# Kernel tuning notes

Hardware: AMD Instinct MI355X
Metric: run time of the kernel (lower is better)

Reference implementation:

```python
import jax, jax.numpy as jnp
import numpy as np

N_EMBD = 1024
COND = 1024
N_HEAD = 16
B, N, NTOK = 4, 2048, 2048


def setup_inputs() -> dict:
    key = jax.random.key(0)
    ks = jax.random.split(key, 10)
    s = 0.02
    return {
        "x": jax.random.normal(ks[0], (B, N, N_EMBD), jnp.float32),
        "encoder_output": jax.random.normal(ks[1], (B, NTOK, COND), jnp.float32),
        "Wq": jax.random.normal(ks[2], (N_EMBD, N_EMBD), jnp.float32) * s,
        "bq": jnp.zeros((N_EMBD,), jnp.float32),
        "Wk": jax.random.normal(ks[3], (N_EMBD, COND), jnp.float32) * s,
        "bk": jnp.zeros((N_EMBD,), jnp.float32),
        "Wv": jax.random.normal(ks[4], (N_EMBD, COND), jnp.float32) * s,
        "bv": jnp.zeros((N_EMBD,), jnp.float32),
        "Wp": jax.random.normal(ks[5], (N_EMBD, N_EMBD), jnp.float32) * s,
        "bp": jnp.zeros((N_EMBD,), jnp.float32),
    }


def reference(x, encoder_output, Wq, bq, Wk, bk, Wv, bv, Wp, bp):
    Bx, Nx, C = x.shape
    H = N_HEAD
    D = C // H
    # projections (torch Linear: y = x @ W^T + b)
    q = (x @ Wq.T + bq).reshape(Bx, Nx, H, D)               # b n h d
    k = (encoder_output @ Wk.T + bk).reshape(Bx, -1, H, D)  # b t h d
    v = (encoder_output @ Wv.T + bv).reshape(Bx, -1, H, D)
    scale = 1.0 / jnp.sqrt(jnp.asarray(D, x.dtype))
    att = jnp.einsum("bnhd,bthd->bhnt", q, k) * scale
    att = jax.nn.softmax(att, axis=-1)
    y = jnp.einsum("bhnt,bthd->bnhd", att, v).reshape(Bx, Nx, C)
    y = y @ Wp.T + bp  # dropout is identity at inference (p effectively 0)
    return y
```

## Files before the change

kernel.cpp:

```cpp
#include <hip/hip_runtime.h>

typedef short bf16x8 __attribute__((ext_vector_type(8)));
typedef float f32x4 __attribute__((ext_vector_type(4)));
typedef unsigned int u32x2 __attribute__((ext_vector_type(2)));

#define AS1 __attribute__((address_space(1)))
#define AS3 __attribute__((address_space(3)))

__device__ __forceinline__ void gld16(void* lds, const void* g) {
  __builtin_amdgcn_global_load_lds((const AS1 unsigned int*)g,
                                   (AS3 unsigned int*)lds, 16, 0, 0);
}

__device__ __forceinline__ unsigned short f2bf(float f) {
  union { float f; unsigned int u; } c; c.f = f;
  return (unsigned short)((c.u + 0x7FFFu + ((c.u >> 16) & 1u)) >> 16);
}

__device__ __forceinline__ unsigned short cvt1(float x) {
  unsigned int r;
  asm("v_cvt_pk_bf16_f32 %0, %1, %1" : "=v"(r) : "v"(x));
  return (unsigned short)r;
}

__device__ __forceinline__ unsigned int cvtpk(float lo, float hi) {
  unsigned int r;
  asm("v_cvt_pk_bf16_f32 %0, %1, %2" : "=v"(r) : "v"(lo), "v"(hi));
  return r;
}

__global__ void cvt_kernel(const float4* __restrict__ in0,
                           const float4* __restrict__ in1,
                           ushort4* __restrict__ out0,
                           ushort4* __restrict__ out1, int n4) {
  const float4* in = blockIdx.y ? in1 : in0;
  ushort4* out = blockIdx.y ? out1 : out0;
  int i = blockIdx.x * blockDim.x + threadIdx.x;
  int stride = gridDim.x * blockDim.x;
  for (; i < n4; i += stride) {
    float4 v = in[i];
    ushort4 o;
    o.x = f2bf(v.x); o.y = f2bf(v.y); o.z = f2bf(v.z); o.w = f2bf(v.w);
    out[i] = o;
  }
}

__global__ void cvtw_kernel(const float4* w0, const float4* w1,
                            const float4* w2, const float4* w3,
                            ushort4* o0, ushort4* o1, ushort4* o2, ushort4* o3,
                            int n4) {
  const float4* in; ushort4* out;
  switch (blockIdx.y) {
    case 0: in = w0; out = o0; break;
    case 1: in = w1; out = o1; break;
    case 2: in = w2; out = o2; break;
    default: in = w3; out = o3; break;
  }
  int i = blockIdx.x * blockDim.x + threadIdx.x;
  int stride = gridDim.x * blockDim.x;
  for (; i < n4; i += stride) {
    float4 v = in[i];
    ushort4 o;
    o.x = f2bf(v.x); o.y = f2bf(v.y); o.z = f2bf(v.z); o.w = f2bf(v.w);
    out[i] = o;
  }
}

__global__ __launch_bounds__(256) void gemm_qkv_kernel(
    const unsigned short* __restrict__ Xb,
    const unsigned short* __restrict__ Eb,
    const unsigned short* __restrict__ Wqb,
    const unsigned short* __restrict__ Wkb,
    const unsigned short* __restrict__ Wvb,
    const float* __restrict__ bq,
    const float* __restrict__ bk,
    const float* __restrict__ bv,
    unsigned short* __restrict__ Qw,
    unsigned short* __restrict__ Kw,
    unsigned short* __restrict__ VTw,
    float qscale)
{
  __shared__ alignas(16) unsigned short As[2][4 * 128 * 8];
  __shared__ alignas(16) unsigned short Bs[2][4 * 128 * 8];

  const int bid = blockIdx.x;
  const int o = (bid & 7) * 192 + (bid >> 3);
  const int xx = o % 24;
  const int yy = o / 24;
  const int sec = xx >> 3;
  const int nx = xx & 7;

  const unsigned short* A = (sec == 0) ? Xb : Eb;
  const unsigned short* W = (sec == 0) ? Wqb : (sec == 1) ? Wkb : Wvb;
  const float* bias = (sec == 0) ? bq : (sec == 1) ? bk : bv;

  const int K = 1024, N = 1024;
  const int tid = threadIdx.x;
  const int lane = tid & 63;
  const int w = tid >> 6;
  const int wr = (w >> 1) * 64;
  const int wc = (w & 1) * 64;
  const int lrow = lane & 15;
  const int lk = lane >> 4;
  const long m0 = (long)yy * 128;
  const long n0 = (long)nx * 128;

  f32x4 acc[4][4] = {};

  const int c0 = tid, c1 = tid + 256;
  const unsigned short* Ag0 = A + (m0 + (c0 & 127)) * (long)K + (c0 >> 7) * 8;
  const unsigned short* Ag1 = A + (m0 + (c1 & 127)) * (long)K + (c1 >> 7) * 8;
  const unsigned short* Wg0 = W + (n0 + (c0 & 127)) * (long)K + (c0 >> 7) * 8;
  const unsigned short* Wg1 = W + (n0 + (c1 & 127)) * (long)K + (c1 >> 7) * 8;

  const int arow = wr + lrow;
  const int brow = wc + lrow;
  const int nt = K >> 5;

  gld16(As[0] + c0 * 8, Ag0);
  gld16(As[0] + c1 * 8, Ag1);
  gld16(Bs[0] + c0 * 8, Wg0);
  gld16(Bs[0] + c1 * 8, Wg1);

  int cur = 0;
  for (int t = 0; t < nt; ++t) {
    __syncthreads();
    if (t + 1 < nt) {
      const int kt = (t + 1) * 32;
      gld16(As[cur ^ 1] + c0 * 8, Ag0 + kt);
      gld16(As[cur ^ 1] + c1 * 8, Ag1 + kt);
      gld16(Bs[cur ^ 1] + c0 * 8, Wg0 + kt);
      gld16(Bs[cur ^ 1] + c1 * 8, Wg1 + kt);
    }
    const unsigned short* as = As[cur];
    const unsigned short* bs = Bs[cur];
    bf16x8 af[4], bfr[4];
#pragma unroll
    for (int i = 0; i < 4; ++i)
      af[i] = *(const bf16x8*)(as + (lk * 128 + arow + i * 16) * 8);
#pragma unroll
    for (int j = 0; j < 4; ++j)
      bfr[j] = *(const bf16x8*)(bs + (lk * 128 + brow + j * 16) * 8);
    if (sec != 2) {
#pragma unroll
      for (int i = 0; i < 4; ++i)
#pragma unroll
        for (int j = 0; j < 4; ++j)
          acc[i][j] = __builtin_amdgcn_mfma_f32_16x16x32_bf16(af[i], bfr[j], acc[i][j], 0, 0, 0);
    } else {
#pragma unroll
      for (int i = 0; i < 4; ++i)
#pragma unroll
        for (int j = 0; j < 4; ++j)
          acc[i][j] = __builtin_amdgcn_mfma_f32_16x16x32_bf16(bfr[i], af[j], acc[i][j], 0, 0, 0);
    }
    cur ^= 1;
  }

  if (sec != 2) {
    unsigned short* out = (sec == 0) ? Qw : Kw;
    const float scale = (sec == 0) ? qscale : 1.0f;
#pragma unroll
    for (int j = 0; j < 4; ++j) {
      const long col = n0 + wc + j * 16 + lrow;
      const float bv_ = bias[col];
#pragma unroll
      for (int i = 0; i < 4; ++i)
#pragma unroll
        for (int r = 0; r < 4; ++r) {
          const long row = m0 + wr + i * 16 + lk * 4 + r;
          out[row * (long)N + col] = cvt1((acc[i][j][r] + bv_) * scale);
        }
    }
  } else {
#pragma unroll
    for (int i = 0; i < 4; ++i)
#pragma unroll
      for (int r = 0; r < 4; ++r) {
        const long feat = n0 + wc + i * 16 + lk * 4 + r;
        const float bv_ = bias[feat];
#pragma unroll
        for (int j = 0; j < 4; ++j) {
          const long col = m0 + wr + j * 16 + lrow;
          VTw[feat * 8192 + col] = cvt1(acc[i][j][r] + bv_);
        }
      }
  }
}

__global__ __launch_bounds__(256) void gemm_p_kernel(
    const unsigned short* __restrict__ A,
    const unsigned short* __restrict__ W,
    const float* __restrict__ bias,
    float* __restrict__ outF)
{
  __shared__ alignas(16) unsigned short As[2][4 * 128 * 8];
  __shared__ alignas(16) unsigned short Bs[2][4 * 128 * 8];

  const int bid = blockIdx.x;
  const int o = (bid & 7) * 64 + (bid >> 3);
  const int nx = o & 7;
  const int yy = o >> 3;

  const int K = 1024, N = 1024;
  const int tid = threadIdx.x;
  const int lane = tid & 63;
  const int w = tid >> 6;
  const int wr = (w >> 1) * 64;
  const int wc = (w & 1) * 64;
  const int lrow = lane & 15;
  const int lk = lane >> 4;
  const long m0 = (long)yy * 128;
  const long n0 = (long)nx * 128;

  f32x4 acc[4][4] = {};

  const int c0 = tid, c1 = tid + 256;
  const unsigned short* Ag0 = A + (m0 + (c0 & 127)) * (long)K + (c0 >> 7) * 8;
  const unsigned short* Ag1 = A + (m0 + (c1 & 127)) * (long)K + (c1 >> 7) * 8;
  const unsigned short* Wg0 = W + (n0 + (c0 & 127)) * (long)K + (c0 >> 7) * 8;
  const unsigned short* Wg1 = W + (n0 + (c1 & 127)) * (long)K + (c1 >> 7) * 8;

  const int arow = wr + lrow;
  const int brow = wc + lrow;
  const int nt = K >> 5;

  gld16(As[0] + c0 * 8, Ag0);
  gld16(As[0] + c1 * 8, Ag1);
  gld16(Bs[0] + c0 * 8, Wg0);
  gld16(Bs[0] + c1 * 8, Wg1);

  int cur = 0;
  for (int t = 0; t < nt; ++t) {
    __syncthreads();
    if (t + 1 < nt) {
      const int kt = (t + 1) * 32;
      gld16(As[cur ^ 1] + c0 * 8, Ag0 + kt);
      gld16(As[cur ^ 1] + c1 * 8, Ag1 + kt);
      gld16(Bs[cur ^ 1] + c0 * 8, Wg0 + kt);
      gld16(Bs[cur ^ 1] + c1 * 8, Wg1 + kt);
    }
    const unsigned short* as = As[cur];
    const unsigned short* bs = Bs[cur];
    bf16x8 af[4], bfr[4];
#pragma unroll
    for (int i = 0; i < 4; ++i)
      af[i] = *(const bf16x8*)(as + (lk * 128 + arow + i * 16) * 8);
#pragma unroll
    for (int j = 0; j < 4; ++j)
      bfr[j] = *(const bf16x8*)(bs + (lk * 128 + brow + j * 16) * 8);
#pragma unroll
    for (int i = 0; i < 4; ++i)
#pragma unroll
      for (int j = 0; j < 4; ++j)
        acc[i][j] = __builtin_amdgcn_mfma_f32_16x16x32_bf16(af[i], bfr[j], acc[i][j], 0, 0, 0);
    cur ^= 1;
  }

#pragma unroll
  for (int j = 0; j < 4; ++j) {
    const long col = n0 + wc + j * 16 + lrow;
    const float bv_ = bias[col];
#pragma unroll
    for (int i = 0; i < 4; ++i)
#pragma unroll
      for (int r = 0; r < 4; ++r) {
        const long row = m0 + wr + i * 16 + lk * 4 + r;
        outF[row * (long)N + col] = acc[i][j][r] + bv_;
      }
  }
}

__global__ __launch_bounds__(256) void attn_kernel(
    const unsigned short* __restrict__ Q,
    const unsigned short* __restrict__ K,
    const unsigned short* __restrict__ VT,
    unsigned short* __restrict__ Y)
{
  __shared__ alignas(16) unsigned short Ks[2][8 * 64 * 8];
  __shared__ alignas(16) unsigned short Vt[2][64 * 64];
  __shared__ alignas(16) unsigned short Ps[128 * 72];

  const int tid = threadIdx.x;
  const int lane = tid & 63;
  const int w = tid >> 6;
  const int lrow = lane & 15;
  const int lk = lane >> 4;

  const int id = blockIdx.x;
  const int r8 = id & 7;
  const int s5 = id >> 3;
  const int qt = s5 & 15;
  const int bh = r8 + 8 * (s5 >> 4);
  const int h = bh & 15, b = bh >> 4;
  const long C = 1024, T = 2048, NQ = 2048;

  const unsigned short* Qg = Q + ((long)b * NQ + qt * 128) * C + h * 64;
  const unsigned short* Kg0 = K + (long)b * T * C + h * 64;
  const unsigned short* Vg0 = VT + (long)(h * 64) * 8192 + b * 2048;

  {
    int c = tid;
    gld16(Ks[0] + c * 8, Kg0 + (long)(c & 63) * C + (c >> 6) * 8);
    c = tid + 256;
    gld16(Ks[0] + c * 8, Kg0 + (long)(c & 63) * C + (c >> 6) * 8);
    c = tid;
    gld16(Vt[0] + c * 8, Vg0 + (long)(c >> 3) * 8192 + (((c & 7) ^ ((c >> 3) & 7)) * 8));
    c = tid + 256;
    gld16(Vt[0] + c * 8, Vg0 + (long)(c >> 3) * 8192 + (((c & 7) ^ ((c >> 3) & 7)) * 8));
  }
  bf16x8 qf[2][2];
#pragma unroll
  for (int f = 0; f < 2; ++f)
#pragma unroll
    for (int kk = 0; kk < 2; ++kk)
      qf[f][kk] = *(const bf16x8*)(Qg + (long)(f * 64 + w * 16 + lrow) * C + (kk * 4 + lk) * 8);

  bf16x8 ones;
#pragma unroll
  for (int e = 0; e < 8; ++e) ones[e] = (short)0x3F80;

  __syncthreads();

  f32x4 oA[4] = {}, oB[4] = {};
  f32x4 olA = {}, olB = {};
  float mrA = 0.f, mrB = 0.f;
  int cur = 0;

  const int qrow0 = w * 16 + lrow;

  for (int kt = 0; kt < (int)T; kt += 64) {
    const bool more = (kt + 64 < (int)T);
    if (more) {
      int c = tid;
      gld16(Ks[cur ^ 1] + c * 8, Kg0 + (long)(kt + 64 + (c & 63)) * C + (c >> 6) * 8);
      gld16(Vt[cur ^ 1] + c * 8,
            Vg0 + (long)(c >> 3) * 8192 + kt + 64 + (((c & 7) ^ ((c >> 3) & 7)) * 8));
      c = tid + 256;
      gld16(Ks[cur ^ 1] + c * 8, Kg0 + (long)(kt + 64 + (c & 63)) * C + (c >> 6) * 8);
      gld16(Vt[cur ^ 1] + c * 8,
            Vg0 + (long)(c >> 3) * 8192 + kt + 64 + (((c & 7) ^ ((c >> 3) & 7)) * 8));
    }

    f32x4 sA[4], sB[4];
#pragma unroll
    for (int j = 0; j < 4; ++j)
#pragma unroll
      for (int r = 0; r < 4; ++r) { sA[j][r] = -mrA; sB[j][r] = -mrB; }

    __builtin_amdgcn_s_setprio(1);
#pragma unroll
    for (int kk = 0; kk < 2; ++kk) {
#pragma unroll
      for (int j = 0; j < 4; ++j) {
        bf16x8 kf = *(const bf16x8*)(Ks[cur] + ((kk * 4 + lk) * 64 + j * 16 + lrow) * 8);
        sA[j] = __builtin_amdgcn_mfma_f32_16x16x32_bf16(kf, qf[0][kk], sA[j], 0, 0, 0);
        sB[j] = __builtin_amdgcn_mfma_f32_16x16x32_bf16(kf, qf[1][kk], sB[j], 0, 0, 0);
      }
    }
    __builtin_amdgcn_s_setprio(0);

    float pmA, pmB;
    {
      float a = fmaxf(fmaxf(fmaxf(sA[0][0], sA[0][1]), fmaxf(sA[0][2], sA[0][3])),
                      fmaxf(fmaxf(sA[1][0], sA[1][1]), fmaxf(sA[1][2], sA[1][3])));
      float b2 = fmaxf(fmaxf(fmaxf(sA[2][0], sA[2][1]), fmaxf(sA[2][2], sA[2][3])),
                       fmaxf(fmaxf(sA[3][0], sA[3][1]), fmaxf(sA[3][2], sA[3][3])));
      pmA = fmaxf(a, b2);
      pmA = fmaxf(pmA, __shfl_xor(pmA, 16));
      pmA = fmaxf(pmA, __shfl_xor(pmA, 32));
      float c2 = fmaxf(fmaxf(fmaxf(sB[0][0], sB[0][1]), fmaxf(sB[0][2], sB[0][3])),
                       fmaxf(fmaxf(sB[1][0], sB[1][1]), fmaxf(sB[1][2], sB[1][3])));
      float d2 = fmaxf(fmaxf(fmaxf(sB[2][0], sB[2][1]), fmaxf(sB[2][2], sB[2][3])),
                       fmaxf(fmaxf(sB[3][0], sB[3][1]), fmaxf(sB[3][2], sB[3][3])));
      pmB = fmaxf(c2, d2);
      pmB = fmaxf(pmB, __shfl_xor(pmB, 16));
      pmB = fmaxf(pmB, __shfl_xor(pmB, 32));
    }
    if (__any(fmaxf(pmA, pmB) > 8.0f)) {
      const float dmA = fmaxf(pmA, 0.f);
      const float alA = __builtin_amdgcn_exp2f(-dmA);
      mrA += dmA; olA *= alA;
      const float dmB = fmaxf(pmB, 0.f);
      const float alB = __builtin_amdgcn_exp2f(-dmB);
      mrB += dmB; olB *= alB;
#pragma unroll
      for (int j = 0; j < 4; ++j) {
        oA[j] *= alA;
        oB[j] *= alB;
#pragma unroll
        for (int r = 0; r < 4; ++r) { sA[j][r] -= dmA; sB[j][r] -= dmB; }
      }
    }
#pragma unroll
    for (int j = 0; j < 4; ++j) {
      float p0 = __builtin_amdgcn_exp2f(sA[j][0]);
      float p1 = __builtin_amdgcn_exp2f(sA[j][1]);
      float p2 = __builtin_amdgcn_exp2f(sA[j][2]);
      float p3 = __builtin_amdgcn_exp2f(sA[j][3]);
      u32x2 pk;
      pk.x = cvtpk(p0, p1);
      pk.y = cvtpk(p2, p3);
      *(u32x2*)(Ps + qrow0 * 72 + j * 16 + lk * 4) = pk;
    }
#pragma unroll
    for (int j = 0; j < 4; ++j) {
      float p0 = __builtin_amdgcn_exp2f(sB[j][0]);
      float p1 = __builtin_amdgcn_exp2f(sB[j][1]);
      float p2 = __builtin_amdgcn_exp2f(sB[j][2]);
      float p3 = __builtin_amdgcn_exp2f(sB[j][3]);
      u32x2 pk;
      pk.x = cvtpk(p0, p1);
      pk.y = cvtpk(p2, p3);
      *(u32x2*)(Ps + (64 + qrow0) * 72 + j * 16 + lk * 4) = pk;
    }

    const unsigned short* vt = Vt[cur];
    __builtin_amdgcn_s_setprio(1);
#pragma unroll
    for (int kk = 0; kk < 2; ++kk) {
      bf16x8 pa0 = *(const bf16x8*)(Ps + qrow0 * 72 + kk * 32 + lk * 8);
      bf16x8 pa1 = *(const bf16x8*)(Ps + (64 + qrow0) * 72 + kk * 32 + lk * 8);
      olA = __builtin_amdgcn_mfma_f32_16x16x32_bf16(ones, pa0, olA, 0, 0, 0);
      olB = __builtin_amdgcn_mfma_f32_16x16x32_bf16(ones, pa1, olB, 0, 0, 0);
#pragma unroll
      for (int j = 0; j < 4; ++j) {
        const int d = j * 16 + lrow;
        bf16x8 vb = *(const bf16x8*)(vt + d * 64 + ((((kk * 4 + lk) ^ (d & 7)) & 7) << 3));
        oA[j] = __builtin_amdgcn_mfma_f32_16x16x32_bf16(vb, pa0, oA[j], 0, 0, 0);
        oB[j] = __builtin_amdgcn_mfma_f32_16x16x32_bf16(vb, pa1, oB[j], 0, 0, 0);
      }
    }
    __builtin_amdgcn_s_setprio(0);

    cur ^= 1;
    __syncthreads();
  }

  unsigned short* Yg = Y + ((long)b * NQ + qt * 128) * C + h * 64;
  const float linvA = 1.f / olA[0];
  const float linvB = 1.f / olB[0];
#pragma unroll
  for (int j = 0; j < 4; ++j) {
    u32x2 pk;
    pk.x = cvtpk(oA[j][0] * linvA, oA[j][1] * linvA);
    pk.y = cvtpk(oA[j][2] * linvA, oA[j][3] * linvA);
    *(u32x2*)(Yg + (long)qrow0 * C + j * 16 + lk * 4) = pk;
    pk.x = cvtpk(oB[j][0] * linvB, oB[j][1] * linvB);
    pk.y = cvtpk(oB[j][2] * linvB, oB[j][3] * linvB);
    *(u32x2*)(Yg + (long)(64 + qrow0) * C + j * 16 + lk * 4) = pk;
  }
}

extern "C" void kernel_launch(void* const* d_in, const int* in_sizes, int n_in,
                              void* d_out, int out_size, void* d_ws, size_t ws_size,
                              hipStream_t stream) {
  (void)in_sizes; (void)n_in; (void)out_size; (void)ws_size;
  const float* x   = (const float*)d_in[0];
  const float* enc = (const float*)d_in[1];
  const float* Wq  = (const float*)d_in[2];
  const float* bq  = (const float*)d_in[3];
  const float* Wk  = (const float*)d_in[4];
  const float* bk  = (const float*)d_in[5];
  const float* Wv  = (const float*)d_in[6];
  const float* bv  = (const float*)d_in[7];
  const float* Wp  = (const float*)d_in[8];
  const float* bp  = (const float*)d_in[9];

  const long M = 4L * 2048;
  const long C = 1024;

  char* ws = (char*)d_ws;
  size_t off = 0;
  auto alloc = [&](size_t bytes) {
    char* p = ws + off;
    off += (bytes + 255) & ~(size_t)255;
    return p;
  };
  unsigned short* Xb  = (unsigned short*)alloc(M * C * 2);
  unsigned short* Eb  = (unsigned short*)alloc(M * C * 2);
  unsigned short* Wqb = (unsigned short*)alloc(C * C * 2);
  unsigned short* Wkb = (unsigned short*)alloc(C * C * 2);
  unsigned short* Wvb = (unsigned short*)alloc(C * C * 2);
  unsigned short* Wpb = (unsigned short*)alloc(C * C * 2);
  unsigned short* Qw  = (unsigned short*)alloc(M * C * 2);
  unsigned short* Kw  = (unsigned short*)alloc(M * C * 2);
  unsigned short* VTw = (unsigned short*)alloc(M * C * 2);
  unsigned short* Yb  = (unsigned short*)alloc(M * C * 2);

  {
    int n4 = (int)(M * C / 4);
    int blocks = (n4 + 255) / 256; if (blocks > 2048) blocks = 2048;
    cvt_kernel<<<dim3(blocks, 2), 256, 0, stream>>>(
        (const float4*)x, (const float4*)enc, (ushort4*)Xb, (ushort4*)Eb, n4);
    int w4 = (int)(C * C / 4);
    cvtw_kernel<<<dim3(1024, 4), 256, 0, stream>>>(
        (const float4*)Wq, (const float4*)Wk, (const float4*)Wv, (const float4*)Wp,
        (ushort4*)Wqb, (ushort4*)Wkb, (ushort4*)Wvb, (ushort4*)Wpb, w4);
  }

  const float qscale = 0.125f * 1.44269504088896f;
  gemm_qkv_kernel<<<1536, 256, 0, stream>>>(
      Xb, Eb, Wqb, Wkb, Wvb, bq, bk, bv, Qw, Kw, VTw, qscale);

  attn_kernel<<<1024, 256, 0, stream>>>(Qw, Kw, VTw, Yb);

  gemm_p_kernel<<<512, 256, 0, stream>>>(Yb, Wpb, bp, (float*)d_out);
}
```

Baseline: 292.2 us.

## Split attention over key dimension into two partitions with a combine kernel

```diff
diff --git a/kernel.cpp b/kernel.cpp
--- a/kernel.cpp
+++ b/kernel.cpp
@@ -3,6 +3,7 @@
 typedef short bf16x8 __attribute__((ext_vector_type(8)));
 typedef float f32x4 __attribute__((ext_vector_type(4)));
 typedef unsigned int u32x2 __attribute__((ext_vector_type(2)));
+typedef unsigned int u32x4 __attribute__((ext_vector_type(4)));
 
 #define AS1 __attribute__((address_space(1)))
 #define AS3 __attribute__((address_space(3)))
@@ -27,6 +28,11 @@
   unsigned int r;
   asm("v_cvt_pk_bf16_f32 %0, %1, %2" : "=v"(r) : "v"(lo), "v"(hi));
   return r;
+}
+
+__device__ __forceinline__ float bf2f(unsigned short u) {
+  union { unsigned int u; float f; } c; c.u = ((unsigned int)u) << 16;
+  return c.f;
 }
 
 __global__ void cvt_kernel(const float4* __restrict__ in0,
@@ -275,7 +281,8 @@
     const unsigned short* __restrict__ Q,
     const unsigned short* __restrict__ K,
     const unsigned short* __restrict__ VT,
-    unsigned short* __restrict__ Y)
+    unsigned short* __restrict__ Op,
+    float2* __restrict__ Lm)
 {
   __shared__ alignas(16) unsigned short Ks[2][8 * 64 * 8];
   __shared__ alignas(16) unsigned short Vt[2][64 * 64];
@@ -289,11 +296,14 @@
 
   const int id = blockIdx.x;
   const int r8 = id & 7;
-  const int s5 = id >> 3;
-  const int qt = s5 & 15;
-  const int bh = r8 + 8 * (s5 >> 4);
+  const int qt = (id >> 3) & 15;
+  const int sp = (id >> 7) & 1;
+  const int s = id >> 8;
+  const int bh = r8 + 8 * s;
   const int h = bh & 15, b = bh >> 4;
   const long C = 1024, T = 2048, NQ = 2048;
+  const int kt0 = sp * 1024;
+  const int ktEnd = kt0 + 1024;
 
   const unsigned short* Qg = Q + ((long)b * NQ + qt * 128) * C + h * 64;
   const unsigned short* Kg0 = K + (long)b * T * C + h * 64;
@@ -301,13 +311,13 @@
 
   {
     int c = tid;
-    gld16(Ks[0] + c * 8, Kg0 + (long)(c & 63) * C + (c >> 6) * 8);
+    gld16(Ks[0] + c * 8, Kg0 + (long)(kt0 + (c & 63)) * C + (c >> 6) * 8);
     c = tid + 256;
-    gld16(Ks[0] + c * 8, Kg0 + (long)(c & 63) * C + (c >> 6) * 8);
+    gld16(Ks[0] + c * 8, Kg0 + (long)(kt0 + (c & 63)) * C + (c >> 6) * 8);
     c = tid;
-    gld16(Vt[0] + c * 8, Vg0 + (long)(c >> 3) * 8192 + (((c & 7) ^ ((c >> 3) & 7)) * 8));
+    gld16(Vt[0] + c * 8, Vg0 + (long)(c >> 3) * 8192 + kt0 + (((c & 7) ^ ((c >> 3) & 7)) * 8));
     c = tid + 256;
-    gld16(Vt[0] + c * 8, Vg0 + (long)(c >> 3) * 8192 + (((c & 7) ^ ((c >> 3) & 7)) * 8));
+    gld16(Vt[0] + c * 8, Vg0 + (long)(c >> 3) * 8192 + kt0 + (((c & 7) ^ ((c >> 3) & 7)) * 8));
   }
   bf16x8 qf[2][2];
 #pragma unroll
@@ -329,8 +339,8 @@
 
   const int qrow0 = w * 16 + lrow;
 
-  for (int kt = 0; kt < (int)T; kt += 64) {
-    const bool more = (kt + 64 < (int)T);
+  for (int kt = kt0; kt < ktEnd; kt += 64) {
+    const bool more = (kt + 64 < ktEnd);
     if (more) {
       int c = tid;
       gld16(Ks[cur ^ 1] + c * 8, Kg0 + (long)(kt + 64 + (c & 63)) * C + (c >> 6) * 8);
@@ -437,19 +447,60 @@
     __syncthreads();
   }
 
-  unsigned short* Yg = Y + ((long)b * NQ + qt * 128) * C + h * 64;
-  const float linvA = 1.f / olA[0];
-  const float linvB = 1.f / olB[0];
+  const long base = ((long)sp * 64 + bh) * 2048;
+  const long qlA = base + qt * 128 + qrow0;
+  const long qlB = qlA + 64;
 #pragma unroll
   for (int j = 0; j < 4; ++j) {
     u32x2 pk;
-    pk.x = cvtpk(oA[j][0] * linvA, oA[j][1] * linvA);
-    pk.y = cvtpk(oA[j][2] * linvA, oA[j][3] * linvA);
-    *(u32x2*)(Yg + (long)qrow0 * C + j * 16 + lk * 4) = pk;
-    pk.x = cvtpk(oB[j][0] * linvB, oB[j][1] * linvB);
-    pk.y = cvtpk(oB[j][2] * linvB, oB[j][3] * linvB);
-    *(u32x2*)(Yg + (long)(64 + qrow0) * C + j * 16 + lk * 4) = pk;
-  }
+    pk.x = cvtpk(oA[j][0], oA[j][1]);
+    pk.y = cvtpk(oA[j][2], oA[j][3]);
+    *(u32x2*)(Op + qlA * 64 + j * 16 + lk * 4) = pk;
+    pk.x = cvtpk(oB[j][0], oB[j][1]);
+    pk.y = cvtpk(oB[j][2], oB[j][3]);
+    *(u32x2*)(Op + qlB * 64 + j * 16 + lk * 4) = pk;
+  }
+  if (lk == 0) {
+    Lm[qlA] = make_float2(olA[0], mrA);
+    Lm[qlB] = make_float2(olB[0], mrB);
+  }
+}
+
+__global__ __launch_bounds__(256) void attn_combine_kernel(
+    const unsigned short* __restrict__ Op,
+    const float2* __restrict__ Lm,
+    unsigned short* __restrict__ Y)
+{
+  const int t = blockIdx.x * 256 + threadIdx.x;
+  const int d0 = t & 7;
+  const int ql = (t >> 3) & 2047;
+  const int bh = t >> 14;
+  const long row = (long)bh * 2048 + ql;
+  const float2 lm0 = Lm[row];
+  const float2 lm1 = Lm[131072 + row];
+  const float m = fmaxf(lm0.y, lm1.y);
+  const float w0 = __builtin_amdgcn_exp2f(lm0.y - m);
+  const float w1 = __builtin_amdgcn_exp2f(lm1.y - m);
+  const float dn = 1.f / (lm0.x * w0 + lm1.x * w1);
+  const float c0 = w0 * dn, c1 = w1 * dn;
+  bf16x8 o0 = *(const bf16x8*)(Op + row * 64 + d0 * 8);
+  bf16x8 o1 = *(const bf16x8*)(Op + (131072L + row) * 64 + d0 * 8);
+  u32x4 pk;
+  float v0, v1;
+  v0 = bf2f((unsigned short)o0[0]) * c0 + bf2f((unsigned short)o1[0]) * c1;
+  v1 = bf2f((unsigned short)o0[1]) * c0 + bf2f((unsigned short)o1[1]) * c1;
+  pk.x = cvtpk(v0, v1);
+  v0 = bf2f((unsigned short)o0[2]) * c0 + bf2f((unsigned short)o1[2]) * c1;
+  v1 = bf2f((unsigned short)o0[3]) * c0 + bf2f((unsigned short)o1[3]) * c1;
+  pk.y = cvtpk(v0, v1);
+  v0 = bf2f((unsigned short)o0[4]) * c0 + bf2f((unsigned short)o1[4]) * c1;
+  v1 = bf2f((unsigned short)o0[5]) * c0 + bf2f((unsigned short)o1[5]) * c1;
+  pk.z = cvtpk(v0, v1);
+  v0 = bf2f((unsigned short)o0[6]) * c0 + bf2f((unsigned short)o1[6]) * c1;
+  v1 = bf2f((unsigned short)o0[7]) * c0 + bf2f((unsigned short)o1[7]) * c1;
+  pk.w = cvtpk(v0, v1);
+  const int b = bh >> 4, h = bh & 15;
+  *(u32x4*)(Y + ((long)b * 2048 + ql) * 1024 + h * 64 + d0 * 8) = pk;
 }
 
 extern "C" void kernel_launch(void* const* d_in, const int* in_sizes, int n_in,
@@ -487,6 +538,9 @@
   unsigned short* Kw  = (unsigned short*)alloc(M * C * 2);
   unsigned short* VTw = (unsigned short*)alloc(M * C * 2);
   unsigned short* Yb  = (unsigned short*)alloc(M * C * 2);
+  float2* Lm = (float2*)alloc(2L * 64 * 2048 * sizeof(float2));
+
+  unsigned short* Op = Xb;
 
   {
     int n4 = (int)(M * C / 4);
@@ -503,7 +557,8 @@
   gemm_qkv_kernel<<<1536, 256, 0, stream>>>(
       Xb, Eb, Wqb, Wkb, Wvb, bq, bk, bv, Qw, Kw, VTw, qscale);
 
-  attn_kernel<<<1024, 256, 0, stream>>>(Qw, Kw, VTw, Yb);
+  attn_kernel<<<2048, 256, 0, stream>>>(Qw, Kw, VTw, Op, Lm);
+  attn_combine_kernel<<<4096, 256, 0, stream>>>(Op, Lm, Yb);
 
   gemm_p_kernel<<<512, 256, 0, stream>>>(Yb, Wpb, bp, (float*)d_out);
 }
```

Result: no change. 287.7 us (-1.6%).
